# Optimization experiments

Hardware: AMD Instinct MI355X
Metric: run time of the kernel (lower is better)

## Reference

```python
import jax, jax.numpy as jnp
import numpy as np

EPS = 1e-08


def conv(x, w, b, stride):
    y = jax.lax.conv_general_dilated(x, w, (stride, stride), 'VALID',
                                     dimension_numbers=('NCHW', 'OIHW', 'NCHW'))
    return y + b[None, :, None, None]


def cnn(x, p):
    x = jax.nn.relu(conv(x, p['c1w'], p['c1b'], 4))
    x = jax.nn.relu(conv(x, p['c2w'], p['c2b'], 2))
    x = jax.nn.relu(conv(x, p['c3w'], p['c3b'], 1))
    x = x.reshape(x.shape[0], -1)  # [B, 3136]
    return jax.nn.relu(x @ p['fcw'] + p['fcb'])  # [B, 256]


def mrn_distance(x, y):
    # x: [B,1,D], y: [1,B,D]
    d = x.shape[-1]
    max_component = jnp.max(jax.nn.relu(x[..., :d // 2] - y[..., :d // 2]), axis=-1)
    l2_component = jnp.sqrt(jnp.sum(jnp.square(x[..., d // 2:] - y[..., d // 2:]), axis=-1) + EPS)
    return max_component + l2_component


def setup_inputs() -> dict:
    key = jax.random.key(0)
    ks = jax.random.split(key, 20)
    B, C, H, W = 512, 4, 84, 84
    F, D = 256, 64
    flat = 7 * 7 * 64  # conv output for 84x84

    def w(k, shape, fan_in):
        return jax.random.normal(k, shape, jnp.float32) * (1.0 / np.sqrt(fan_in))

    return {
        'curr_obs': jax.random.uniform(ks[0], (B, C, H, W), jnp.float32),
        'next_obs': jax.random.uniform(ks[1], (B, C, H, W), jnp.float32),
        'c1w': w(ks[2], (32, C, 8, 8), C * 64), 'c1b': jnp.zeros((32,), jnp.float32),
        'c2w': w(ks[3], (64, 32, 4, 4), 32 * 16), 'c2b': jnp.zeros((64,), jnp.float32),
        'c3w': w(ks[4], (64, 64, 3, 3), 64 * 9), 'c3b': jnp.zeros((64,), jnp.float32),
        'fcw': w(ks[5], (flat, F), flat), 'fcb': jnp.zeros((F,), jnp.float32),
        'e1w': w(ks[6], (F, F), F), 'e1b': jnp.zeros((F,), jnp.float32),
        'e2w': w(ks[7], (F, D), F), 'e2b': jnp.zeros((D,), jnp.float32),
        'pw1': w(ks[8], (F, F), F), 'pb1': jnp.zeros((F,), jnp.float32),
        'pw2': w(ks[9], (F, 1), F), 'pb2': jnp.zeros((1,), jnp.float32),
    }


def reference(curr_obs, next_obs, c1w, c1b, c2w, c2b, c3w, c3b, fcw, fcb,
              e1w, e1b, e2w, e2b, pw1, pb1, pw2, pb2):
    p = dict(c1w=c1w, c1b=c1b, c2w=c2w, c2b=c2b, c3w=c3w, c3b=c3b, fcw=fcw, fcb=fcb)
    curr_f = cnn(curr_obs, p)
    next_f = cnn(next_obs, p)
    encode = lambda f: jax.nn.relu(f @ e1w + e1b) @ e2w + e2b
    phi_x = encode(curr_f)                                   # [B, D]
    phi_y = encode(next_f)                                   # [B, D]
    c_y = jax.nn.relu(next_f @ pw1 + pb1) @ pw2 + pb2        # [B, 1]

    # energy_fn == 'mrn_pot': potential bias minus pairwise MRN distance
    logits = c_y.T - mrn_distance(phi_x[:, None], phi_y[None, :])  # [B, B]

    B = logits.shape[0]
    # infonce: cross-entropy with labels arange(B) == -mean diag(log_softmax)
    logp = jax.nn.log_softmax(logits, axis=1)
    contrastive_loss = -jnp.mean(jnp.diagonal(logp))
    logsumexp_loss = jnp.mean(jax.nn.logsumexp(logits + 1e-06, axis=1) ** 2)
    total_loss = contrastive_loss + 0.1 * logsumexp_loss
    return total_loss
```

## Files before the change

### kernel.cpp

```cpp
#include <hip/hip_runtime.h>
#include <math.h>

typedef __attribute__((ext_vector_type(8))) short bf16x8;
typedef __attribute__((ext_vector_type(4))) float f32x4;

static __device__ __forceinline__ ushort f2bf(float x) {
    union { float f; unsigned u; } a; a.f = x;
    unsigned r = a.u + 0x7fff + ((a.u >> 16) & 1);
    return (ushort)(r >> 16);
}

__global__ __launch_bounds__(256) void repack_all_k(const float* __restrict__ c1w,
                                                    const float* __restrict__ c2w,
                                                    const float* __restrict__ c3w,
                                                    const float* __restrict__ fcw,
                                                    ushort* __restrict__ wp1,
                                                    ushort* __restrict__ wp2,
                                                    ushort* __restrict__ wp3,
                                                    ushort* __restrict__ wfc) {
    const int blk = blockIdx.x;
    if (blk < 32) {
        const int t = blk * 256 + threadIdx.x;
        const int j = t & 7, l = (t >> 3) & 63, kk = (t >> 9) & 7, ot = t >> 12;
        const int oc = ot * 16 + (l & 15);
        const int k  = kk * 32 + ((l >> 4) * 8) + j;
        wp1[t] = f2bf(c1w[oc * 256 + k]);
    } else if (blk < 160) {
        const int t = (blk - 32) * 256 + threadIdx.x;
        const int j = t & 7, l = (t >> 3) & 63, kk = (t >> 9) & 15, wv = t >> 13;
        const int oc = wv * 16 + (l & 15);
        const int k  = kk * 32 + ((l >> 4) * 8) + j;
        wp2[t] = f2bf(c2w[oc * 512 + k]);
    } else if (blk < 304) {
        const int t = (blk - 160) * 256 + threadIdx.x;
        const int j = t & 7, l = (t >> 3) & 63, kk = (t >> 9) & 1;
        const int ot = (t >> 10) & 3, kp = t >> 12;
        const int oc = ot * 16 + (l & 15);
        const int ic = kk * 32 + ((l >> 4) * 8) + j;
        wp3[t] = f2bf(c3w[(oc * 64 + ic) * 9 + kp]);
    } else {
        const int t = (blk - 304) * 256 + threadIdx.x;
        const int n = t / 3136, kp = t % 3136;
        const int pos = kp >> 6, oc = kp & 63;
        wfc[t] = f2bf(fcw[(oc * 49 + pos) * 256 + n]);
    }
}

__global__ __launch_bounds__(256) void conv1_mfma_k(const float* __restrict__ curr,
                                                    const float* __restrict__ nxt,
                                                    const ushort* __restrict__ wpack,
                                                    const float* __restrict__ bias,
                                                    ushort* __restrict__ y) {
    __shared__ ushort xt[4 * 44 * 84];
    const int tid = threadIdx.x;
    const int pass = blockIdx.x >> 10;
    const int rb = blockIdx.x & 1023;
    const int b = rb >> 1, sup = rb & 1;

    const float* xb = (pass ? nxt : curr) + (size_t)b * 28224;
    const int ih0 = sup * 40;
    for (int i = tid; i < 3696; i += 256) {
        const int row = i / 21, col = i % 21;
        const int ic = row / 44, rr = row % 44;
        const float4 v = *(const float4*)(xb + ic * 7056 + (ih0 + rr) * 84 + col * 4);
        ushort4 u; u.x = f2bf(v.x); u.y = f2bf(v.y); u.z = f2bf(v.z); u.w = f2bf(v.w);
        *(ushort4*)(xt + (ic * 44 + rr) * 84 + col * 4) = u;
    }
    __syncthreads();

    const int wv = tid >> 6, l = tid & 63, q = l >> 4, col = l & 15;

    bf16x8 a[2][8];
    const bf16x8* wp = (const bf16x8*)wpack;
    #pragma unroll
    for (int ot = 0; ot < 2; ++ot)
        #pragma unroll
        for (int kk = 0; kk < 8; ++kk) a[ot][kk] = wp[(ot * 8 + kk) * 64 + l];

    float bv[2][4];
    #pragma unroll
    for (int ot = 0; ot < 2; ++ot)
        #pragma unroll
        for (int r = 0; r < 4; ++r) bv[ot][r] = bias[ot * 16 + q * 4 + r];

    const size_t ybase = ((size_t)(pass * 512 + b)) * 32 * 400;

    for (int t = wv; t < 13; t += 4) {
        const int lraw = t * 16 + col;
        const int lpos = lraw < 200 ? lraw : 199;
        const int ohl = lpos / 20, ow = lpos % 20;
        f32x4 acc0 = {0.f, 0.f, 0.f, 0.f}, acc1 = {0.f, 0.f, 0.f, 0.f};
        #pragma unroll
        for (int kk = 0; kk < 8; ++kk) {
            const int ickh = kk * 4 + q;
            const int ic = ickh >> 3, kh = ickh & 7;
            const int base = ic * 3696 + (ohl * 4 + kh) * 84 + ow * 4;
            union { uint2 u2[2]; bf16x8 v; } f;
            f.u2[0] = *(const uint2*)(xt + base);
            f.u2[1] = *(const uint2*)(xt + base + 4);
            acc0 = __builtin_amdgcn_mfma_f32_16x16x32_bf16(a[0][kk], f.v, acc0, 0, 0, 0);
            acc1 = __builtin_amdgcn_mfma_f32_16x16x32_bf16(a[1][kk], f.v, acc1, 0, 0, 0);
        }
        if (lraw < 200) {
            const int pos = sup * 200 + lraw;
            #pragma unroll
            for (int r = 0; r < 4; ++r) {
                y[ybase + (size_t)(q * 4 + r) * 400 + pos]      = f2bf(fmaxf(acc0[r] + bv[0][r], 0.f));
                y[ybase + (size_t)(16 + q * 4 + r) * 400 + pos] = f2bf(fmaxf(acc1[r] + bv[1][r], 0.f));
            }
        }
    }
}

__global__ __launch_bounds__(256) void conv23_mfma_k(const ushort* __restrict__ x,
                                                     const ushort* __restrict__ wp2g,
                                                     const float* __restrict__ b2,
                                                     const ushort* __restrict__ wp3g,
                                                     const float* __restrict__ b3,
                                                     ushort* __restrict__ y) {
    __shared__ ushort xt[12800];
    __shared__ ushort xt2[81 * 68];
    const int tid = threadIdx.x;
    const int img = blockIdx.x;

    const uint4* xg = (const uint4*)(x + (size_t)img * 12800);
    for (int i = tid; i < 1600; i += 256) *(uint4*)(xt + i * 8) = xg[i];
    __syncthreads();

    const int wv = tid >> 6, l = tid & 63, quad = l >> 4, col = l & 15;

    {
        int ohs[6], ows[6];
        #pragma unroll
        for (int t = 0; t < 6; ++t) {
            int pos = t * 16 + col; if (pos > 80) pos = 80;
            ohs[t] = pos / 9; ows[t] = pos % 9;
        }
        const int ic_off = quad >> 1;
        const int kh2    = (quad & 1) * 2;

        float bias_v[4];
        #pragma unroll
        for (int r2 = 0; r2 < 4; ++r2) bias_v[r2] = b2[wv * 16 + quad * 4 + r2];

        f32x4 acc[6];
        #pragma unroll
        for (int t = 0; t < 6; ++t) acc[t] = (f32x4){0.f, 0.f, 0.f, 0.f};

        const bf16x8* wp = (const bf16x8*)wp2g;
        for (int kk = 0; kk < 16; ++kk) {
            const bf16x8 a = wp[(wv * 16 + kk) * 64 + l];
            const int ic = kk * 2 + ic_off;
            #pragma unroll
            for (int t = 0; t < 6; ++t) {
                const int base = ic * 400 + (ohs[t] * 2 + kh2) * 20 + ows[t] * 2;
                const unsigned* p0 = (const unsigned*)(xt + base);
                const unsigned* p1 = (const unsigned*)(xt + base + 20);
                union { unsigned u[4]; bf16x8 v; } f;
                f.u[0] = p0[0]; f.u[1] = p0[1];
                f.u[2] = p1[0]; f.u[3] = p1[1];
                acc[t] = __builtin_amdgcn_mfma_f32_16x16x32_bf16(a, f.v, acc[t], 0, 0, 0);
            }
        }
        #pragma unroll
        for (int t = 0; t < 6; ++t) {
            const int pos = t * 16 + col;
            if (pos < 81) {
                ushort4 u;
                u.x = f2bf(fmaxf(acc[t][0] + bias_v[0], 0.f));
                u.y = f2bf(fmaxf(acc[t][1] + bias_v[1], 0.f));
                u.z = f2bf(fmaxf(acc[t][2] + bias_v[2], 0.f));
                u.w = f2bf(fmaxf(acc[t][3] + bias_v[3], 0.f));
                *(ushort4*)(xt2 + pos * 68 + wv * 16 + quad * 4) = u;
            }
        }
    }
    __syncthreads();

    {
        int ohs[4], ows[4];
        #pragma unroll
        for (int pt = 0; pt < 4; ++pt) {
            int pos = pt * 16 + col; if (pos > 48) pos = 48;
            ohs[pt] = pos / 7; ows[pt] = pos % 7;
        }
        float bv[4];
        #pragma unroll
        for (int r = 0; r < 4; ++r) bv[r] = b3[wv * 16 + quad * 4 + r];

        f32x4 acc[4];
        #pragma unroll
        for (int pt = 0; pt < 4; ++pt) acc[pt] = (f32x4){0.f, 0.f, 0.f, 0.f};

        const bf16x8* wp = (const bf16x8*)wp3g;
        #pragma unroll
        for (int kp = 0; kp < 9; ++kp) {
            const int kh = kp / 3, kw = kp % 3;
            #pragma unroll
            for (int kk = 0; kk < 2; ++kk) {
                const bf16x8 a = wp[((kp * 4 + wv) * 2 + kk) * 64 + l];
                #pragma unroll
                for (int pt = 0; pt < 4; ++pt) {
                    const int rpos = (ohs[pt] + kh) * 9 + (ows[pt] + kw);
                    const int base = rpos * 68 + kk * 32 + quad * 8;
                    union { uint2 u2[2]; bf16x8 v; } f;
                    f.u2[0] = *(const uint2*)(xt2 + base);
                    f.u2[1] = *(const uint2*)(xt2 + base + 4);
                    acc[pt] = __builtin_amdgcn_mfma_f32_16x16x32_bf16(a, f.v, acc[pt], 0, 0, 0);
                }
            }
        }
        #pragma unroll
        for (int pt = 0; pt < 4; ++pt) {
            const int pos = pt * 16 + col;
            if (pos < 49) {
                ushort4 u;
                u.x = f2bf(fmaxf(acc[pt][0] + bv[0], 0.f));
                u.y = f2bf(fmaxf(acc[pt][1] + bv[1], 0.f));
                u.z = f2bf(fmaxf(acc[pt][2] + bv[2], 0.f));
                u.w = f2bf(fmaxf(acc[pt][3] + bv[3], 0.f));
                *(ushort4*)(y + (size_t)img * 3136 + pos * 64 + wv * 16 + quad * 4) = u;
            }
        }
    }
}

__global__ __launch_bounds__(256) void fc_mfma_k(const ushort* __restrict__ a3,
                                                 const ushort* __restrict__ wfc,
                                                 const float* __restrict__ bias,
                                                 float* __restrict__ feat) {
    const int tid = threadIdx.x;
    const int pass = blockIdx.x >> 6;
    const int gw = (blockIdx.x & 63) * 4 + (tid >> 6);
    const int l = tid & 63, q = l >> 4, col = l & 15;
    const int mtile = gw >> 3, np = gw & 7;

    const ushort* arow = a3 + (size_t)pass * 1605632 + (size_t)(mtile * 16 + col) * 3136;
    const ushort* brow0 = wfc + (size_t)(np * 32 + col) * 3136;
    const ushort* brow1 = brow0 + (size_t)16 * 3136;

    f32x4 acc0 = {0.f, 0.f, 0.f, 0.f}, acc1 = {0.f, 0.f, 0.f, 0.f};
    #pragma unroll 2
    for (int kk = 0; kk < 98; ++kk) {
        const int ko = kk * 32 + q * 8;
        const bf16x8 av = *(const bf16x8*)(arow + ko);
        const bf16x8 b0 = *(const bf16x8*)(brow0 + ko);
        const bf16x8 b1 = *(const bf16x8*)(brow1 + ko);
        acc0 = __builtin_amdgcn_mfma_f32_16x16x32_bf16(av, b0, acc0, 0, 0, 0);
        acc1 = __builtin_amdgcn_mfma_f32_16x16x32_bf16(av, b1, acc1, 0, 0, 0);
    }

    float* fb = feat + (size_t)pass * 131072;
    #pragma unroll
    for (int r = 0; r < 4; ++r) {
        const int m = mtile * 16 + q * 4 + r;
        const int n0 = np * 32 + col, n1 = n0 + 16;
        fb[m * 256 + n0] = fmaxf(acc0[r] + bias[n0], 0.f);
        fb[m * 256 + n1] = fmaxf(acc1[r] + bias[n1], 0.f);
    }
}

__global__ __launch_bounds__(256) void heads_k(const float* __restrict__ feat,
                                               const float* __restrict__ e1w,
                                               const float* __restrict__ e1b,
                                               const float* __restrict__ e2w,
                                               const float* __restrict__ e2b,
                                               const float* __restrict__ pw1,
                                               const float* __restrict__ pb1,
                                               const float* __restrict__ pw2,
                                               const float* __restrict__ pb2,
                                               float* __restrict__ phi_x,
                                               float* __restrict__ phiYT,
                                               float* __restrict__ c_y,
                                               float* __restrict__ accbuf) {
    __shared__ float fc[2][256], fn[2][256];
    __shared__ float h1c[2][256], h1n[2][256], hp[2][256];
    const int tid = threadIdx.x;
    const int b0 = blockIdx.x * 2;

    if (blockIdx.x == 0 && tid < 4) accbuf[tid] = 0.f;

    for (int i = tid; i < 512; i += 256) {
        const int rr = i >> 8, c = i & 255;
        fc[rr][c] = feat[(b0 + rr) * 256 + c];
        fn[rr][c] = feat[131072 + (b0 + rr) * 256 + c];
    }
    __syncthreads();

    float ac0 = e1b[tid], ac1 = ac0;
    float an0 = ac0, an1 = ac0;
    float ap0 = pb1[tid], ap1 = ap0;
    for (int k = 0; k < 256; ++k) {
        const float we = e1w[k * 256 + tid];
        const float wpv = pw1[k * 256 + tid];
        ac0 += fc[0][k] * we;  ac1 += fc[1][k] * we;
        an0 += fn[0][k] * we;  an1 += fn[1][k] * we;
        ap0 += fn[0][k] * wpv; ap1 += fn[1][k] * wpv;
    }
    h1c[0][tid] = fmaxf(ac0, 0.f); h1c[1][tid] = fmaxf(ac1, 0.f);
    h1n[0][tid] = fmaxf(an0, 0.f); h1n[1][tid] = fmaxf(an1, 0.f);
    hp[0][tid]  = fmaxf(ap0, 0.f); hp[1][tid]  = fmaxf(ap1, 0.f);
    __syncthreads();

    const int wave = tid >> 6, lane = tid & 63;
    if (wave == 0) {
        #pragma unroll
        for (int rr = 0; rr < 2; ++rr) {
            float s = e2b[lane];
            for (int k = 0; k < 256; ++k) s += h1c[rr][k] * e2w[k * 64 + lane];
            phi_x[(b0 + rr) * 64 + lane] = s;
        }
    } else if (wave == 1) {
        #pragma unroll
        for (int rr = 0; rr < 2; ++rr) {
            float s = e2b[lane];
            for (int k = 0; k < 256; ++k) s += h1n[rr][k] * e2w[k * 64 + lane];
            phiYT[lane * 512 + b0 + rr] = s;
        }
    } else {
        const int rr = wave - 2;
        float s = 0.f;
        #pragma unroll
        for (int q2 = 0; q2 < 4; ++q2) s += hp[rr][lane * 4 + q2] * pw2[lane * 4 + q2];
        #pragma unroll
        for (int off = 32; off > 0; off >>= 1) s += __shfl_down(s, off);
        if (lane == 0) c_y[b0 + rr] = s + pb2[0];
    }
}

__global__ __launch_bounds__(256) void row_lse_loss_k(const float* __restrict__ phi_x,
                                                      const float* __restrict__ phiYT,
                                                      const float* __restrict__ c_y,
                                                      float* __restrict__ accbuf,
                                                      float* __restrict__ out) {
    const int i = blockIdx.x, tid = threadIdx.x;
    __shared__ float px[64];
    __shared__ float red[256];
    __shared__ float sdiag;
    if (tid < 64) px[tid] = phi_x[i * 64 + tid];
    __syncthreads();

    float lg[2];
    #pragma unroll
    for (int q = 0; q < 2; ++q) {
        const int j = tid + q * 256;
        float m = -1e30f;
        #pragma unroll 8
        for (int k = 0; k < 32; ++k) m = fmaxf(m, px[k] - phiYT[k * 512 + j]);
        const float maxc = fmaxf(m, 0.f);
        float s = 0.f;
        #pragma unroll 8
        for (int k = 32; k < 64; ++k) {
            const float d = px[k] - phiYT[k * 512 + j];
            s += d * d;
        }
        lg[q] = c_y[j] - (maxc + sqrtf(s + 1e-8f));
    }
    if ((i & 255) == tid) sdiag = lg[i >> 8];

    red[tid] = fmaxf(lg[0], lg[1]);
    __syncthreads();
    for (int s = 128; s > 0; s >>= 1) {
        if (tid < s) red[tid] = fmaxf(red[tid], red[tid + s]);
        __syncthreads();
    }
    const float m = red[0];
    __syncthreads();
    red[tid] = expf(lg[0] - m) + expf(lg[1] - m);
    __syncthreads();
    for (int s = 128; s > 0; s >>= 1) {
        if (tid < s) red[tid] += red[tid + s];
        __syncthreads();
    }

    if (tid == 0) {
        const float lse = m + logf(red[0]);
        const float l2 = lse + 1e-6f;
        atomicAdd(&accbuf[0], lse - sdiag);
        atomicAdd(&accbuf[1], l2 * l2);
        __threadfence();
        const unsigned old = atomicAdd((unsigned*)&accbuf[2], 1u);
        if (old == 511u) {
            __threadfence();
            const float s1 = atomicAdd(&accbuf[0], 0.f);
            const float s2 = atomicAdd(&accbuf[1], 0.f);
            out[0] = s1 / 512.f + 0.1f * (s2 / 512.f);
        }
    }
}

extern "C" void kernel_launch(void* const* d_in, const int* in_sizes, int n_in,
                              void* d_out, int out_size, void* d_ws, size_t ws_size,
                              hipStream_t stream) {
    const float* curr = (const float*)d_in[0];
    const float* nxt  = (const float*)d_in[1];
    const float* c1w  = (const float*)d_in[2];
    const float* c1b  = (const float*)d_in[3];
    const float* c2w  = (const float*)d_in[4];
    const float* c2b  = (const float*)d_in[5];
    const float* c3w  = (const float*)d_in[6];
    const float* c3b  = (const float*)d_in[7];
    const float* fcw  = (const float*)d_in[8];
    const float* fcb  = (const float*)d_in[9];
    const float* e1w  = (const float*)d_in[10];
    const float* e1b  = (const float*)d_in[11];
    const float* e2w  = (const float*)d_in[12];
    const float* e2b  = (const float*)d_in[13];
    const float* pw1  = (const float*)d_in[14];
    const float* pb1  = (const float*)d_in[15];
    const float* pw2  = (const float*)d_in[16];
    const float* pb2  = (const float*)d_in[17];

    ushort* a1  = (ushort*)d_ws;
    ushort* a3  = a1 + 13107200;
    ushort* wp1 = a3 + 3211264;
    ushort* wp2 = wp1 + 8192;
    ushort* wp3 = wp2 + 32768;
    ushort* wfc = wp3 + 36864;
    float*  feat  = (float*)(wfc + 802816);
    float*  phi_x = feat + 262144;
    float*  phiYT = phi_x + 32768;
    float*  c_y   = phiYT + 32768;
    float*  acc   = c_y + 512;

    repack_all_k<<<3440, 256, 0, stream>>>(c1w, c2w, c3w, fcw, wp1, wp2, wp3, wfc);
    conv1_mfma_k<<<2048, 256, 0, stream>>>(curr, nxt, wp1, c1b, a1);
    conv23_mfma_k<<<1024, 256, 0, stream>>>(a1, wp2, c2b, wp3, c3b, a3);
    fc_mfma_k<<<128, 256, 0, stream>>>(a3, wfc, fcb, feat);
    heads_k<<<256, 256, 0, stream>>>(feat, e1w, e1b, e2w, e2b, pw1, pb1, pw2, pb2,
                                     phi_x, phiYT, c_y, acc);
    row_lse_loss_k<<<512, 256, 0, stream>>>(phi_x, phiYT, c_y, acc, (float*)d_out);
}
```

Before: 315.6 us.

## Fuse conv1 into conv2/conv3 kernel, keeping conv1 output in shared memory

Merges the conv1 kernel into the conv2/conv3 kernel, so each 512-thread block computes all three convolutions for one image. The conv1 activation stays in LDS instead of making a 26 MB bf16 round trip through global memory, and conv1's input staging buffer is reused for the conv2 output. conv2 and conv3 work is split across 8 waves as output-channel tiles by spatial halves. The cost is more LDS per block (about 57 KB), which may limit occupancy, plus a serial two-pass conv1 phase per block. Conv1 weights are also now read from global memory inside the loop rather than preloaded into registers.

```diff
diff --git a/kernel.cpp b/kernel.cpp
--- a/kernel.cpp
+++ b/kernel.cpp
@@ -46,161 +46,150 @@
     }
 }
 
-__global__ __launch_bounds__(256) void conv1_mfma_k(const float* __restrict__ curr,
-                                                    const float* __restrict__ nxt,
-                                                    const ushort* __restrict__ wpack,
-                                                    const float* __restrict__ bias,
-                                                    ushort* __restrict__ y) {
-    __shared__ ushort xt[4 * 44 * 84];
+__global__ __launch_bounds__(512, 4) void convs_k(const float* __restrict__ curr,
+                                                  const float* __restrict__ nxt,
+                                                  const ushort* __restrict__ wp1g,
+                                                  const float* __restrict__ b1,
+                                                  const ushort* __restrict__ wp2g,
+                                                  const float* __restrict__ b2,
+                                                  const ushort* __restrict__ wp3g,
+                                                  const float* __restrict__ b3,
+                                                  ushort* __restrict__ a3out) {
+    __shared__ ushort stage[4 * 44 * 84];
+    __shared__ ushort xt1[12800];
     const int tid = threadIdx.x;
-    const int pass = blockIdx.x >> 10;
-    const int rb = blockIdx.x & 1023;
-    const int b = rb >> 1, sup = rb & 1;
-
-    const float* xb = (pass ? nxt : curr) + (size_t)b * 28224;
-    const int ih0 = sup * 40;
-    for (int i = tid; i < 3696; i += 256) {
-        const int row = i / 21, col = i % 21;
-        const int ic = row / 44, rr = row % 44;
-        const float4 v = *(const float4*)(xb + ic * 7056 + (ih0 + rr) * 84 + col * 4);
-        ushort4 u; u.x = f2bf(v.x); u.y = f2bf(v.y); u.z = f2bf(v.z); u.w = f2bf(v.w);
-        *(ushort4*)(xt + (ic * 44 + rr) * 84 + col * 4) = u;
-    }
-    __syncthreads();
-
-    const int wv = tid >> 6, l = tid & 63, q = l >> 4, col = l & 15;
-
-    bf16x8 a[2][8];
-    const bf16x8* wp = (const bf16x8*)wpack;
+    const int img = blockIdx.x;
+    const float* xb = (img >= 512 ? nxt + (size_t)(img - 512) * 28224
+                                  : curr + (size_t)img * 28224);
+
+    const int w8 = tid >> 6;
+    const int l = tid & 63, quad = l >> 4, col = l & 15;
+    const bf16x8* wp1f = (const bf16x8*)wp1g;
+    const bf16x8* wp2f = (const bf16x8*)wp2g;
+    const bf16x8* wp3f = (const bf16x8*)wp3g;
+
+    float bv1[2][4];
     #pragma unroll
     for (int ot = 0; ot < 2; ++ot)
         #pragma unroll
-        for (int kk = 0; kk < 8; ++kk) a[ot][kk] = wp[(ot * 8 + kk) * 64 + l];
-
-    float bv[2][4];
-    #pragma unroll
-    for (int ot = 0; ot < 2; ++ot)
-        #pragma unroll
-        for (int r = 0; r < 4; ++r) bv[ot][r] = bias[ot * 16 + q * 4 + r];
-
-    const size_t ybase = ((size_t)(pass * 512 + b)) * 32 * 400;
-
-    for (int t = wv; t < 13; t += 4) {
-        const int lraw = t * 16 + col;
-        const int lpos = lraw < 200 ? lraw : 199;
-        const int ohl = lpos / 20, ow = lpos % 20;
-        f32x4 acc0 = {0.f, 0.f, 0.f, 0.f}, acc1 = {0.f, 0.f, 0.f, 0.f};
-        #pragma unroll
-        for (int kk = 0; kk < 8; ++kk) {
-            const int ickh = kk * 4 + q;
-            const int ic = ickh >> 3, kh = ickh & 7;
-            const int base = ic * 3696 + (ohl * 4 + kh) * 84 + ow * 4;
-            union { uint2 u2[2]; bf16x8 v; } f;
-            f.u2[0] = *(const uint2*)(xt + base);
-            f.u2[1] = *(const uint2*)(xt + base + 4);
-            acc0 = __builtin_amdgcn_mfma_f32_16x16x32_bf16(a[0][kk], f.v, acc0, 0, 0, 0);
-            acc1 = __builtin_amdgcn_mfma_f32_16x16x32_bf16(a[1][kk], f.v, acc1, 0, 0, 0);
-        }
-        if (lraw < 200) {
-            const int pos = sup * 200 + lraw;
+        for (int r = 0; r < 4; ++r) bv1[ot][r] = b1[ot * 16 + quad * 4 + r];
+
+    for (int sup = 0; sup < 2; ++sup) {
+        if (sup) __syncthreads();
+        const int ih0 = sup * 40;
+        for (int i = tid; i < 3696; i += 512) {
+            const int row = i / 21, c4 = i % 21;
+            const int ic = row / 44, rr = row % 44;
+            const float4 v = *(const float4*)(xb + ic * 7056 + (ih0 + rr) * 84 + c4 * 4);
+            ushort4 u; u.x = f2bf(v.x); u.y = f2bf(v.y); u.z = f2bf(v.z); u.w = f2bf(v.w);
+            *(ushort4*)(stage + (ic * 44 + rr) * 84 + c4 * 4) = u;
+        }
+        __syncthreads();
+
+        for (int t = w8; t < 13; t += 8) {
+            const int lraw = t * 16 + col;
+            const int lpos = lraw < 200 ? lraw : 199;
+            const int ohl = lpos / 20, ow = lpos % 20;
+            f32x4 acc0 = {0.f, 0.f, 0.f, 0.f}, acc1 = {0.f, 0.f, 0.f, 0.f};
             #pragma unroll
-            for (int r = 0; r < 4; ++r) {
-                y[ybase + (size_t)(q * 4 + r) * 400 + pos]      = f2bf(fmaxf(acc0[r] + bv[0][r], 0.f));
-                y[ybase + (size_t)(16 + q * 4 + r) * 400 + pos] = f2bf(fmaxf(acc1[r] + bv[1][r], 0.f));
-            }
-        }
-    }
-}
-
-__global__ __launch_bounds__(256) void conv23_mfma_k(const ushort* __restrict__ x,
-                                                     const ushort* __restrict__ wp2g,
-                                                     const float* __restrict__ b2,
-                                                     const ushort* __restrict__ wp3g,
-                                                     const float* __restrict__ b3,
-                                                     ushort* __restrict__ y) {
-    __shared__ ushort xt[12800];
-    __shared__ ushort xt2[81 * 68];
-    const int tid = threadIdx.x;
-    const int img = blockIdx.x;
-
-    const uint4* xg = (const uint4*)(x + (size_t)img * 12800);
-    for (int i = tid; i < 1600; i += 256) *(uint4*)(xt + i * 8) = xg[i];
-    __syncthreads();
-
-    const int wv = tid >> 6, l = tid & 63, quad = l >> 4, col = l & 15;
+            for (int kk = 0; kk < 8; ++kk) {
+                const bf16x8 a0 = wp1f[kk * 64 + l];
+                const bf16x8 a1 = wp1f[(8 + kk) * 64 + l];
+                const int ickh = kk * 4 + quad;
+                const int ic = ickh >> 3, kh = ickh & 7;
+                const int base = ic * 3696 + (ohl * 4 + kh) * 84 + ow * 4;
+                union { uint2 u2[2]; bf16x8 v; } f;
+                f.u2[0] = *(const uint2*)(stage + base);
+                f.u2[1] = *(const uint2*)(stage + base + 4);
+                acc0 = __builtin_amdgcn_mfma_f32_16x16x32_bf16(a0, f.v, acc0, 0, 0, 0);
+                acc1 = __builtin_amdgcn_mfma_f32_16x16x32_bf16(a1, f.v, acc1, 0, 0, 0);
+            }
+            if (lraw < 200) {
+                const int pos = sup * 200 + lraw;
+                #pragma unroll
+                for (int r = 0; r < 4; ++r) {
+                    xt1[(quad * 4 + r) * 400 + pos]      = f2bf(fmaxf(acc0[r] + bv1[0][r], 0.f));
+                    xt1[(16 + quad * 4 + r) * 400 + pos] = f2bf(fmaxf(acc1[r] + bv1[1][r], 0.f));
+                }
+            }
+        }
+    }
+    __syncthreads();
+    ushort* xt2 = stage;
 
     {
-        int ohs[6], ows[6];
-        #pragma unroll
-        for (int t = 0; t < 6; ++t) {
-            int pos = t * 16 + col; if (pos > 80) pos = 80;
-            ohs[t] = pos / 9; ows[t] = pos % 9;
+        const int oct = w8 & 3, half = w8 >> 2;
+        int ohs[3], ows[3];
+        #pragma unroll
+        for (int tt = 0; tt < 3; ++tt) {
+            int pos = (half * 3 + tt) * 16 + col; if (pos > 80) pos = 80;
+            ohs[tt] = pos / 9; ows[tt] = pos % 9;
         }
         const int ic_off = quad >> 1;
         const int kh2    = (quad & 1) * 2;
 
         float bias_v[4];
         #pragma unroll
-        for (int r2 = 0; r2 < 4; ++r2) bias_v[r2] = b2[wv * 16 + quad * 4 + r2];
-
-        f32x4 acc[6];
-        #pragma unroll
-        for (int t = 0; t < 6; ++t) acc[t] = (f32x4){0.f, 0.f, 0.f, 0.f};
-
-        const bf16x8* wp = (const bf16x8*)wp2g;
+        for (int r2 = 0; r2 < 4; ++r2) bias_v[r2] = b2[oct * 16 + quad * 4 + r2];
+
+        f32x4 acc[3];
+        #pragma unroll
+        for (int tt = 0; tt < 3; ++tt) acc[tt] = (f32x4){0.f, 0.f, 0.f, 0.f};
+
         for (int kk = 0; kk < 16; ++kk) {
-            const bf16x8 a = wp[(wv * 16 + kk) * 64 + l];
+            const bf16x8 a = wp2f[(oct * 16 + kk) * 64 + l];
             const int ic = kk * 2 + ic_off;
             #pragma unroll
-            for (int t = 0; t < 6; ++t) {
-                const int base = ic * 400 + (ohs[t] * 2 + kh2) * 20 + ows[t] * 2;
-                const unsigned* p0 = (const unsigned*)(xt + base);
-                const unsigned* p1 = (const unsigned*)(xt + base + 20);
+            for (int tt = 0; tt < 3; ++tt) {
+                const int base = ic * 400 + (ohs[tt] * 2 + kh2) * 20 + ows[tt] * 2;
+                const unsigned* p0 = (const unsigned*)(xt1 + base);
+                const unsigned* p1 = (const unsigned*)(xt1 + base + 20);
                 union { unsigned u[4]; bf16x8 v; } f;
                 f.u[0] = p0[0]; f.u[1] = p0[1];
                 f.u[2] = p1[0]; f.u[3] = p1[1];
-                acc[t] = __builtin_amdgcn_mfma_f32_16x16x32_bf16(a, f.v, acc[t], 0, 0, 0);
-            }
-        }
-        #pragma unroll
-        for (int t = 0; t < 6; ++t) {
-            const int pos = t * 16 + col;
+                acc[tt] = __builtin_amdgcn_mfma_f32_16x16x32_bf16(a, f.v, acc[tt], 0, 0, 0);
+            }
+        }
+        __syncthreads();
+        #pragma unroll
+        for (int tt = 0; tt < 3; ++tt) {
+            const int pos = (half * 3 + tt) * 16 + col;
             if (pos < 81) {
                 ushort4 u;
-                u.x = f2bf(fmaxf(acc[t][0] + bias_v[0], 0.f));
-                u.y = f2bf(fmaxf(acc[t][1] + bias_v[1], 0.f));
-                u.z = f2bf(fmaxf(acc[t][2] + bias_v[2], 0.f));
-                u.w = f2bf(fmaxf(acc[t][3] + bias_v[3], 0.f));
-                *(ushort4*)(xt2 + pos * 68 + wv * 16 + quad * 4) = u;
+                u.x = f2bf(fmaxf(acc[tt][0] + bias_v[0], 0.f));
+                u.y = f2bf(fmaxf(acc[tt][1] + bias_v[1], 0.f));
+                u.z = f2bf(fmaxf(acc[tt][2] + bias_v[2], 0.f));
+                u.w = f2bf(fmaxf(acc[tt][3] + bias_v[3], 0.f));
+                *(ushort4*)(xt2 + pos * 68 + oct * 16 + quad * 4) = u;
             }
         }
     }
     __syncthreads();
 
     {
-        int ohs[4], ows[4];
-        #pragma unroll
-        for (int pt = 0; pt < 4; ++pt) {
-            int pos = pt * 16 + col; if (pos > 48) pos = 48;
+        const int oct = w8 & 3, half = w8 >> 2;
+        int ohs[2], ows[2];
+        #pragma unroll
+        for (int pt = 0; pt < 2; ++pt) {
+            int pos = (half * 2 + pt) * 16 + col; if (pos > 48) pos = 48;
             ohs[pt] = pos / 7; ows[pt] = pos % 7;
         }
         float bv[4];
         #pragma unroll
-        for (int r = 0; r < 4; ++r) bv[r] = b3[wv * 16 + quad * 4 + r];
-
-        f32x4 acc[4];
-        #pragma unroll
-        for (int pt = 0; pt < 4; ++pt) acc[pt] = (f32x4){0.f, 0.f, 0.f, 0.f};
-
-        const bf16x8* wp = (const bf16x8*)wp3g;
+        for (int r = 0; r < 4; ++r) bv[r] = b3[oct * 16 + quad * 4 + r];
+
+        f32x4 acc[2];
+        #pragma unroll
+        for (int pt = 0; pt < 2; ++pt) acc[pt] = (f32x4){0.f, 0.f, 0.f, 0.f};
+
         #pragma unroll
         for (int kp = 0; kp < 9; ++kp) {
             const int kh = kp / 3, kw = kp % 3;
             #pragma unroll
             for (int kk = 0; kk < 2; ++kk) {
-                const bf16x8 a = wp[((kp * 4 + wv) * 2 + kk) * 64 + l];
+                const bf16x8 a = wp3f[((kp * 4 + oct) * 2 + kk) * 64 + l];
                 #pragma unroll
-                for (int pt = 0; pt < 4; ++pt) {
+                for (int pt = 0; pt < 2; ++pt) {
                     const int rpos = (ohs[pt] + kh) * 9 + (ows[pt] + kw);
                     const int base = rpos * 68 + kk * 32 + quad * 8;
                     union { uint2 u2[2]; bf16x8 v; } f;
@@ -211,15 +200,15 @@
             }
         }
         #pragma unroll
-        for (int pt = 0; pt < 4; ++pt) {
-            const int pos = pt * 16 + col;
+        for (int pt = 0; pt < 2; ++pt) {
+            const int pos = (half * 2 + pt) * 16 + col;
             if (pos < 49) {
                 ushort4 u;
                 u.x = f2bf(fmaxf(acc[pt][0] + bv[0], 0.f));
                 u.y = f2bf(fmaxf(acc[pt][1] + bv[1], 0.f));
                 u.z = f2bf(fmaxf(acc[pt][2] + bv[2], 0.f));
                 u.w = f2bf(fmaxf(acc[pt][3] + bv[3], 0.f));
-                *(ushort4*)(y + (size_t)img * 3136 + pos * 64 + wv * 16 + quad * 4) = u;
+                *(ushort4*)(a3out + (size_t)img * 3136 + pos * 64 + oct * 16 + quad * 4) = u;
             }
         }
     }
@@ -230,12 +219,11 @@
                                                  const float* __restrict__ bias,
                                                  float* __restrict__ feat) {
     const int tid = threadIdx.x;
-    const int pass = blockIdx.x >> 6;
-    const int gw = (blockIdx.x & 63) * 4 + (tid >> 6);
+    const int gw = blockIdx.x * 4 + (tid >> 6);
     const int l = tid & 63, q = l >> 4, col = l & 15;
     const int mtile = gw >> 3, np = gw & 7;
 
-    const ushort* arow = a3 + (size_t)pass * 1605632 + (size_t)(mtile * 16 + col) * 3136;
+    const ushort* arow = a3 + (size_t)(mtile * 16 + col) * 3136;
     const ushort* brow0 = wfc + (size_t)(np * 32 + col) * 3136;
     const ushort* brow1 = brow0 + (size_t)16 * 3136;
 
@@ -250,13 +238,12 @@
         acc1 = __builtin_amdgcn_mfma_f32_16x16x32_bf16(av, b1, acc1, 0, 0, 0);
     }
 
-    float* fb = feat + (size_t)pass * 131072;
     #pragma unroll
     for (int r = 0; r < 4; ++r) {
         const int m = mtile * 16 + q * 4 + r;
         const int n0 = np * 32 + col, n1 = n0 + 16;
-        fb[m * 256 + n0] = fmaxf(acc0[r] + bias[n0], 0.f);
-        fb[m * 256 + n1] = fmaxf(acc1[r] + bias[n1], 0.f);
+        feat[m * 256 + n0] = fmaxf(acc0[r] + bias[n0], 0.f);
+        feat[m * 256 + n1] = fmaxf(acc1[r] + bias[n1], 0.f);
     }
 }
 
@@ -411,8 +398,7 @@
     const float* pw2  = (const float*)d_in[16];
     const float* pb2  = (const float*)d_in[17];
 
-    ushort* a1  = (ushort*)d_ws;
-    ushort* a3  = a1 + 13107200;
+    ushort* a3  = (ushort*)d_ws;
     ushort* wp1 = a3 + 3211264;
     ushort* wp2 = wp1 + 8192;
     ushort* wp3 = wp2 + 32768;
@@ -424,8 +410,7 @@
     float*  acc   = c_y + 512;
 
     repack_all_k<<<3440, 256, 0, stream>>>(c1w, c2w, c3w, fcw, wp1, wp2, wp3, wfc);
-    conv1_mfma_k<<<2048, 256, 0, stream>>>(curr, nxt, wp1, c1b, a1);
-    conv23_mfma_k<<<1024, 256, 0, stream>>>(a1, wp2, c2b, wp3, c3b, a3);
+    convs_k<<<1024, 512, 0, stream>>>(curr, nxt, wp1, c1b, wp2, c2b, wp3, c3b, a3);
     fc_mfma_k<<<128, 256, 0, stream>>>(a3, wfc, fcb, feat);
     heads_k<<<256, 256, 0, stream>>>(feat, e1w, e1b, e2w, e2b, pw1, pb1, pw2, pb2,
                                      phi_x, phiYT, c_y, acc);
```

Measured after the change: 316.7 us. Within noise of the previous version (+0.4%).
